# Performance work log

Hardware: AMD Instinct MI355X
Metric: run time of the kernel (lower is better)

The kernel has to match this reference:

```python
import jax, jax.numpy as jnp
import numpy as np
from jax import lax

INPUT_DIM = 512
KERNEL_DIM = 3
HEADS = 8
B, L = 16, 1024


def setup_inputs() -> dict:
    key = jax.random.key(0)
    ks = jax.random.split(key, 4)
    fan = INPUT_DIM * KERNEL_DIM
    std = float(np.sqrt(2.0 / (INPUT_DIM + fan)))  # xavier_normal for conv weight
    x = jax.random.normal(ks[0], (B, INPUT_DIM, L), dtype=jnp.float32)
    w0 = jax.random.normal(ks[1], (INPUT_DIM, INPUT_DIM, KERNEL_DIM), dtype=jnp.float32) * std
    w1 = jax.random.normal(ks[2], (INPUT_DIM, INPUT_DIM, KERNEL_DIM), dtype=jnp.float32) * std
    w2 = jax.random.normal(ks[3], (INPUT_DIM, INPUT_DIM, KERNEL_DIM), dtype=jnp.float32) * std
    b0 = jnp.zeros((INPUT_DIM,), jnp.float32)
    b1 = jnp.zeros((INPUT_DIM,), jnp.float32)
    b2 = jnp.zeros((INPUT_DIM,), jnp.float32)
    return {"x": x, "w0": w0, "b0": b0, "w1": w1, "b1": b1, "w2": w2, "b2": b2}


def _conv1d(x, w, b):
    # x: [B, C, L], w: [O, I, K] -> [B, O, L-K+1] (VALID, stride 1)
    y = lax.conv_general_dilated(x, w, window_strides=(1,), padding='VALID',
                                 dimension_numbers=('NCH', 'OIH', 'NCH'))
    return y + b[None, :, None]


def _multihead_attention(q, k, v, input_dim, heads):
    # q,k,v: [B, D, Lp]; chunk along channel dim == reshape to [B, H, Dh, Lp]
    b, d, lp = q.shape
    dh = d // heads
    qh = q.reshape(b, heads, dh, lp)
    kh = k.reshape(b, heads, dh, lp)
    vh = v.reshape(b, heads, dh, lp)
    scale = 1.0 / np.sqrt(input_dim)  # NOTE: original scales by sqrt(full input_dim)
    scores = jnp.einsum('bhdq,bhdk->bhqk', qh, kh) * scale  # [B,H,Lp,Lp]
    attn = jax.nn.softmax(scores, axis=-1)
    out = jnp.einsum('bhqk,bhdk->bhdq', attn, vh)  # [B,H,Dh,Lp]
    return out.reshape(b, d, lp)


def reference(x, w0, b0, w1, b1, w2, b2):
    q = _conv1d(x, w0, b0)
    k = _conv1d(x, w1, b1)
    v = _conv1d(x, w2, b2)
    return _multihead_attention(q, k, v, INPUT_DIM, HEADS)
```

## Files before the change

kernel.cpp:

```cpp
#include <hip/hip_runtime.h>

#define B_SZ 16
#define CIN  512
#define LIN  1024
#define LP   1022
#define HEADS 8
#define DH    64

typedef __attribute__((ext_vector_type(8))) short bf16x8;
typedef __attribute__((ext_vector_type(4))) float f32x4;

__device__ inline unsigned short f2bf(float f) {
    union { float f; unsigned int u; } c; c.f = f;
    unsigned int r = c.u + 0x7FFF + ((c.u >> 16) & 1);
    return (unsigned short)(r >> 16);
}

__device__ __forceinline__ void gl_lds16(const unsigned short* g, unsigned short* l) {
    __builtin_amdgcn_global_load_lds((const __attribute__((address_space(1))) void*)g,
                                     (__attribute__((address_space(3))) void*)l, 16, 0, 0);
}

#define SWZ(G) ((G) ^ (((G) >> 3) & 7))

__global__ __launch_bounds__(256) void xb_cvt_kernel(const float* __restrict__ x,
                                                     unsigned short* __restrict__ xb) {
    __shared__ float sm[64][68];
    const int t  = threadIdx.x;
    const int l0 = blockIdx.x * 64;
    const int i0 = blockIdx.y * 64;
    const int b  = blockIdx.z;
    const float* S = x + ((size_t)b * CIN + i0) * LIN;

    #pragma unroll
    for (int rr = 0; rr < 4; rr++) {
        int idx = rr * 1024 + t * 4;
        int ii = idx >> 6, lj = idx & 63;
        *(float4*)&sm[ii][lj] = *(const float4*)(S + (size_t)ii * LIN + l0 + lj);
    }
    __syncthreads();

    #pragma unroll
    for (int rr = 0; rr < 4; rr++) {
        int idx = rr * 1024 + t * 4;
        int l = idx >> 6, dj = idx & 63;
        ushort4 h;
        h.x = f2bf(sm[dj + 0][l]);
        h.y = f2bf(sm[dj + 1][l]);
        h.z = f2bf(sm[dj + 2][l]);
        h.w = f2bf(sm[dj + 3][l]);
        *(ushort4*)(xb + ((size_t)b * 1024 + l0 + l) * 512 + i0 + dj) = h;
    }
}

__global__ __launch_bounds__(256) void wb_cvt_kernel(const float* __restrict__ w0,
                                                     const float* __restrict__ w1,
                                                     const float* __restrict__ w2,
                                                     unsigned short* __restrict__ wb) {
    const int kk = blockIdx.y;
    int flat = blockIdx.x * 256 + threadIdx.x;
    int i  = flat & 511;
    int oG = flat >> 9;
    int c  = oG >> 9, o = oG & 511;
    const float* w = (c == 0) ? w0 : (c == 1) ? w1 : w2;
    wb[(size_t)kk * 786432 + flat] = f2bf(w[o * 1536 + i * 3 + kk]);
}

__global__ __launch_bounds__(256) void conv_mfma_kernel(
        const unsigned short* __restrict__ xb,
        const unsigned short* __restrict__ wb,
        const float* __restrict__ b0, const float* __restrict__ b1,
        const float* __restrict__ b2,
        unsigned short* __restrict__ Qt, unsigned short* __restrict__ Kt,
        unsigned short* __restrict__ Vt, float qscale) {
    __shared__ unsigned short smem[16896];
    unsigned short* xs = smem;
    unsigned short* ws = smem + 4224;

    const int t    = threadIdx.x;
    const int wave = t >> 6;
    const int lane = t & 63;
    const int col  = lane & 15;
    const int quad = lane >> 4;
    const int wh   = wave >> 1;
    const int wn   = wave & 1;
    const int l0   = blockIdx.x * 128;
    const int o0   = blockIdx.y * 128;
    const int b    = blockIdx.z;

    f32x4 acc[4][4];
    #pragma unroll
    for (int i = 0; i < 4; i++)
        #pragma unroll
        for (int j = 0; j < 4; j++) acc[i][j] = (f32x4){0.f, 0.f, 0.f, 0.f};

    const unsigned short* xrow = xb + (size_t)b * 1024 * 512;

    for (int ic = 0; ic < 512; ic += 32) {
        __syncthreads();

        #pragma unroll
        for (int j = 0; j < 6; j++) {
            int instr = wave * 6 + j;
            int Gg = SWZ(instr * 64 + lane);
            int p = Gg >> 2, q = Gg & 3;
            int kk = p >> 7, orow = p & 127;
            gl_lds16(wb + ((size_t)(kk * 1536 + o0 + orow)) * 512 + ic + q * 8,
                     ws + instr * 512);
        }
        #pragma unroll
        for (int j = 0; j < 2; j++) {
            int instr = wave * 2 + j;
            int Gg = SWZ(instr * 64 + lane);
            int p = Gg >> 2, q = Gg & 3;
            gl_lds16(xrow + (size_t)(l0 + p) * 512 + ic + q * 8,
                     xs + instr * 512);
        }
        if (t < 8) {
            int row = 128 + (t >> 2), sg = t & 3;
            int gl = l0 + row;
            bf16x8 v = (bf16x8){0, 0, 0, 0, 0, 0, 0, 0};
            if (gl < 1024) v = *(const bf16x8*)(xrow + (size_t)gl * 512 + ic + sg * 8);
            *(bf16x8*)&xs[SWZ(512 + t) * 8] = v;
        }
        __syncthreads();

        #pragma unroll
        for (int kk = 0; kk < 3; kk++) {
            bf16x8 af[4], bfr[4];
            #pragma unroll
            for (int ms = 0; ms < 4; ms++) {
                int G = ((kk * 128 + wh * 64 + ms * 16 + col) << 2) | quad;
                af[ms] = *(const bf16x8*)&ws[SWZ(G) * 8];
            }
            #pragma unroll
            for (int ns = 0; ns < 4; ns++) {
                int G = ((wn * 64 + ns * 16 + col + kk) << 2) | quad;
                bfr[ns] = *(const bf16x8*)&xs[SWZ(G) * 8];
            }
            #pragma unroll
            for (int ms = 0; ms < 4; ms++)
                #pragma unroll
                for (int ns = 0; ns < 4; ns++)
                    acc[ms][ns] = __builtin_amdgcn_mfma_f32_16x16x32_bf16(af[ms], bfr[ns], acc[ms][ns], 0, 0, 0);
        }
    }

    const int c = blockIdx.y >> 2;

    if (c < 2) {
        unsigned short* dst = (c == 0) ? Qt : Kt;
        const float* bias   = (c == 0) ? b0 : b1;
        const float sc      = (c == 0) ? qscale : 1.0f;
        const int h = (((o0 & 511) + wh * 64) >> 6) & 7;
        unsigned short* base = dst + (size_t)(b * 8 + h) * 65536;
        #pragma unroll
        for (int ms = 0; ms < 4; ms++) {
            int ob = (o0 & 511) + wh * 64 + ms * 16 + quad * 4;
            float bv[4];
            #pragma unroll
            for (int r = 0; r < 4; r++) bv[r] = bias[ob + r];
            int d0 = ms * 16 + quad * 4;
            #pragma unroll
            for (int ns = 0; ns < 4; ns++) {
                int l = l0 + wn * 64 + ns * 16 + col;
                ushort4 hv;
                hv.x = f2bf((acc[ms][ns][0] + bv[0]) * sc);
                hv.y = f2bf((acc[ms][ns][1] + bv[1]) * sc);
                hv.z = f2bf((acc[ms][ns][2] + bv[2]) * sc);
                hv.w = f2bf((acc[ms][ns][3] + bv[3]) * sc);
                *(ushort4*)(base + (size_t)l * 64 + d0) = hv;
            }
        }
    } else {
        __syncthreads();
        unsigned short* vt = smem;
        #pragma unroll
        for (int ms = 0; ms < 4; ms++) {
            int ob = (o0 & 511) + wh * 64 + ms * 16 + quad * 4;
            #pragma unroll
            for (int ns = 0; ns < 4; ns++) {
                int lc = wn * 64 + ns * 16 + col;
                #pragma unroll
                for (int r = 0; r < 4; r++)
                    vt[(wh * 64 + ms * 16 + quad * 4 + r) * 132 + lc] =
                        f2bf(acc[ms][ns][r] + b2[ob + r]);
            }
        }
        __syncthreads();
        #pragma unroll
        for (int it = 0; it < 8; it++) {
            int flat = it * 2048 + t * 8;
            int row = flat >> 7, colx = flat & 127;
            bf16x8 v = *(const bf16x8*)&vt[row * 132 + colx];
            int og = (o0 & 511) + row;
            int h = og >> 6, d = og & 63;
            *(bf16x8*)(Vt + ((size_t)(b * 8 + h) * 64 + d) * 1024 + l0 + colx) = v;
        }
    }
}

__global__ __launch_bounds__(256, 4) void attn_kernel(
        const unsigned short* __restrict__ Qt,
        const unsigned short* __restrict__ Kt,
        const unsigned short* __restrict__ Vt,
        float* __restrict__ out) {
    __shared__ unsigned short smem[17408];
    unsigned short* Ks = smem;
    unsigned short* Vs = smem + 4096;
    unsigned short* Ps = smem + 8192;

    const int t    = threadIdx.x;
    const int wave = t >> 6;
    const int lane = t & 63;
    const int col  = lane & 15;
    const int quad = lane >> 4;
    const int qb   = blockIdx.x;
    const int bh   = blockIdx.y;

    const size_t base64 = (size_t)bh * 1024 * 64;
    const int q0w = qb * 128 + wave * 32;

    bf16x8 bq[2][2];
    #pragma unroll
    for (int g = 0; g < 2; g++) {
        const unsigned short* qrow = Qt + base64 + (size_t)(q0w + g * 16 + col) * 64;
        bq[g][0] = *(const bf16x8*)(qrow + quad * 8);
        bq[g][1] = *(const bf16x8*)(qrow + 32 + quad * 8);
    }

    const bf16x8 ones = (bf16x8){0x3F80, 0x3F80, 0x3F80, 0x3F80,
                                 0x3F80, 0x3F80, 0x3F80, 0x3F80};

    f32x4 o[2][4];
    #pragma unroll
    for (int g = 0; g < 2; g++)
        #pragma unroll
        for (int d = 0; d < 4; d++) o[g][d] = (f32x4){0.f, 0.f, 0.f, 0.f};
    f32x4 osum[2];
    osum[0] = (f32x4){0.f, 0.f, 0.f, 0.f};
    osum[1] = (f32x4){0.f, 0.f, 0.f, 0.f};

    const unsigned short* kg0 = Kt + base64;
    const unsigned short* vg  = Vt + base64;
    unsigned short* Pw = Ps + wave * 32 * 72;

    for (int kt = 0; kt < 16; kt++) {
        __syncthreads();

        const unsigned short* kg = kg0 + (size_t)kt * 4096;
        #pragma unroll
        for (int j = 0; j < 2; j++) {
            int i = wave + j * 4;
            int G = SWZ(i * 64 + lane);
            gl_lds16(kg + (size_t)G * 8, Ks + i * 512);
            int p = G >> 3, q = G & 7;
            gl_lds16(vg + (size_t)p * 1024 + kt * 64 + q * 8, Vs + i * 512);
        }
        __syncthreads();

        bf16x8 ak[4][2];
        #pragma unroll
        for (int sub = 0; sub < 4; sub++) {
            int rk = sub * 16 + col;
            ak[sub][0] = *(const bf16x8*)&Ks[SWZ(rk * 8 + quad) * 8];
            ak[sub][1] = *(const bf16x8*)&Ks[SWZ(rk * 8 + 4 + quad) * 8];
        }

        #pragma unroll
        for (int g = 0; g < 2; g++) {
            #pragma unroll
            for (int sub = 0; sub < 4; sub++) {
                f32x4 a = (f32x4){0.f, 0.f, 0.f, 0.f};
                a = __builtin_amdgcn_mfma_f32_16x16x32_bf16(ak[sub][0], bq[g][0], a, 0, 0, 0);
                a = __builtin_amdgcn_mfma_f32_16x16x32_bf16(ak[sub][1], bq[g][1], a, 0, 0, 0);
                unsigned int u[4];
                #pragma unroll
                for (int r = 0; r < 4; r++) {
                    union { float f; unsigned int u; } c;
                    c.f = exp2f(a[r]);
                    u[r] = c.u;
                }
                if (kt == 15 && sub == 3 && quad == 3) {
                    u[2] = 0; u[3] = 0;
                }
                uint2 pk;
                pk.x = (u[0] >> 16) | (u[1] & 0xFFFF0000u);
                pk.y = (u[2] >> 16) | (u[3] & 0xFFFF0000u);
                *(uint2*)&Pw[(g * 16 + col) * 72 + sub * 16 + quad * 4] = pk;
            }
        }

        bf16x8 av[4][2];
        #pragma unroll
        for (int dsub = 0; dsub < 4; dsub++) {
            int rd = dsub * 16 + col;
            av[dsub][0] = *(const bf16x8*)&Vs[SWZ(rd * 8 + quad) * 8];
            av[dsub][1] = *(const bf16x8*)&Vs[SWZ(rd * 8 + 4 + quad) * 8];
        }

        #pragma unroll
        for (int g = 0; g < 2; g++) {
            bf16x8 bp0 = *(const bf16x8*)&Pw[(g * 16 + col) * 72 + quad * 8];
            bf16x8 bp1 = *(const bf16x8*)&Pw[(g * 16 + col) * 72 + 32 + quad * 8];
            #pragma unroll
            for (int dsub = 0; dsub < 4; dsub++) {
                o[g][dsub] = __builtin_amdgcn_mfma_f32_16x16x32_bf16(av[dsub][0], bp0, o[g][dsub], 0, 0, 0);
                o[g][dsub] = __builtin_amdgcn_mfma_f32_16x16x32_bf16(av[dsub][1], bp1, o[g][dsub], 0, 0, 0);
            }
            osum[g] = __builtin_amdgcn_mfma_f32_16x16x32_bf16(ones, bp0, osum[g], 0, 0, 0);
            osum[g] = __builtin_amdgcn_mfma_f32_16x16x32_bf16(ones, bp1, osum[g], 0, 0, 0);
        }
    }

    #pragma unroll
    for (int g = 0; g < 2; g++) {
        int q = q0w + g * 16 + col;
        if (q < LP) {
            float inv = 1.0f / osum[g][0];
            #pragma unroll
            for (int dsub = 0; dsub < 4; dsub++) {
                #pragma unroll
                for (int r = 0; r < 4; r++) {
                    int d = dsub * 16 + quad * 4 + r;
                    out[((size_t)bh * 64 + d) * LP + q] = o[g][dsub][r] * inv;
                }
            }
        }
    }
}

extern "C" void kernel_launch(void* const* d_in, const int* in_sizes, int n_in,
                              void* d_out, int out_size, void* d_ws, size_t ws_size,
                              hipStream_t stream) {
    const float* x  = (const float*)d_in[0];
    const float* w0 = (const float*)d_in[1];
    const float* b0 = (const float*)d_in[2];
    const float* w1 = (const float*)d_in[3];
    const float* b1 = (const float*)d_in[4];
    const float* w2 = (const float*)d_in[5];
    const float* b2 = (const float*)d_in[6];
    float* out = (float*)d_out;

    unsigned short* xbp = (unsigned short*)d_ws;
    unsigned short* wbp = xbp + 8388608;
    unsigned short* Qt  = wbp + 2359296;
    unsigned short* Kt  = Qt + 8388608;
    unsigned short* Vt  = Kt + 8388608;

    const float scale = 0.06375870864f;

    xb_cvt_kernel<<<dim3(16, 8, 16), 256, 0, stream>>>(x, xbp);
    wb_cvt_kernel<<<dim3(3072, 3), 256, 0, stream>>>(w0, w1, w2, wbp);
    conv_mfma_kernel<<<dim3(8, 12, 16), 256, 0, stream>>>(xbp, wbp, b0, b1, b2,
                                                          Qt, Kt, Vt, scale);
    attn_kernel<<<dim3(8, 128), 256, 0, stream>>>(Qt, Kt, Vt, out);
}
```

Before: 242.0 us.

## Double-buffer K/V tiles in attention, remap blocks per XCD, add MFMA priority

The attention kernel now prefetches the next K/V tile into a second LDS buffer while computing on the current one, replacing the two per-iteration __syncthreads with a single waitcnt plus barrier. Block indices are remapped so that all query blocks of a given batch-head land on the same XCD, which should improve L2 reuse of K/V. s_setprio raises wave priority around the MFMA groups. LDS use grows from about 34 KB to 50 KB and the occupancy hint drops from 4 to 3 blocks per CU, so there is less latency hiding from resident waves.

```diff
diff --git a/kernel.cpp b/kernel.cpp
--- a/kernel.cpp
+++ b/kernel.cpp
@@ -200,23 +200,25 @@
     }
 }
 
-__global__ __launch_bounds__(256, 4) void attn_kernel(
+__global__ __launch_bounds__(256, 3) void attn_kernel(
         const unsigned short* __restrict__ Qt,
         const unsigned short* __restrict__ Kt,
         const unsigned short* __restrict__ Vt,
         float* __restrict__ out) {
-    __shared__ unsigned short smem[17408];
-    unsigned short* Ks = smem;
-    unsigned short* Vs = smem + 4096;
-    unsigned short* Ps = smem + 8192;
+    __shared__ unsigned short smem[25600];
+    unsigned short* Ps = smem + 16384;
 
     const int t    = threadIdx.x;
     const int wave = t >> 6;
     const int lane = t & 63;
     const int col  = lane & 15;
     const int quad = lane >> 4;
-    const int qb   = blockIdx.x;
-    const int bh   = blockIdx.y;
+
+    const int lin = blockIdx.y * 8 + blockIdx.x;
+    const int xcd = lin & 7;
+    const int idx = lin >> 3;
+    const int qb  = idx >> 4;
+    const int bh  = xcd * 16 + (idx & 15);
 
     const size_t base64 = (size_t)bh * 1024 * 64;
     const int q0w = qb * 128 + wave * 32;
@@ -245,26 +247,50 @@
     const unsigned short* vg  = Vt + base64;
     unsigned short* Pw = Ps + wave * 32 * 72;
 
+    #pragma unroll
+    for (int j = 0; j < 2; j++) {
+        int i = wave + j * 4;
+        int G = SWZ(i * 64 + lane);
+        gl_lds16(kg0 + (size_t)G * 8, smem + i * 512);
+        int p = G >> 3, q = G & 7;
+        gl_lds16(vg + (size_t)p * 1024 + q * 8, smem + 4096 + i * 512);
+    }
+    asm volatile("s_waitcnt vmcnt(0)" ::: "memory");
+    __builtin_amdgcn_s_barrier();
+    asm volatile("" ::: "memory");
+
+    int cur = 0;
     for (int kt = 0; kt < 16; kt++) {
-        __syncthreads();
-
-        const unsigned short* kg = kg0 + (size_t)kt * 4096;
-        #pragma unroll
-        for (int j = 0; j < 2; j++) {
-            int i = wave + j * 4;
-            int G = SWZ(i * 64 + lane);
-            gl_lds16(kg + (size_t)G * 8, Ks + i * 512);
-            int p = G >> 3, q = G & 7;
-            gl_lds16(vg + (size_t)p * 1024 + kt * 64 + q * 8, Vs + i * 512);
-        }
-        __syncthreads();
+        if (kt < 15) {
+            const unsigned short* kg = kg0 + (size_t)(kt + 1) * 4096;
+            unsigned short* Kb = smem + (cur ^ 1) * 8192;
+            #pragma unroll
+            for (int j = 0; j < 2; j++) {
+                int i = wave + j * 4;
+                int G = SWZ(i * 64 + lane);
+                gl_lds16(kg + (size_t)G * 8, Kb + i * 512);
+                int p = G >> 3, q = G & 7;
+                gl_lds16(vg + (size_t)p * 1024 + (kt + 1) * 64 + q * 8,
+                         Kb + 4096 + i * 512);
+            }
+        }
+
+        const unsigned short* Ksb = smem + cur * 8192;
+        const unsigned short* Vsb = Ksb + 4096;
 
         bf16x8 ak[4][2];
         #pragma unroll
         for (int sub = 0; sub < 4; sub++) {
             int rk = sub * 16 + col;
-            ak[sub][0] = *(const bf16x8*)&Ks[SWZ(rk * 8 + quad) * 8];
-            ak[sub][1] = *(const bf16x8*)&Ks[SWZ(rk * 8 + 4 + quad) * 8];
+            ak[sub][0] = *(const bf16x8*)&Ksb[SWZ(rk * 8 + quad) * 8];
+            ak[sub][1] = *(const bf16x8*)&Ksb[SWZ(rk * 8 + 4 + quad) * 8];
+        }
+        bf16x8 av[4][2];
+        #pragma unroll
+        for (int dsub = 0; dsub < 4; dsub++) {
+            int rd = dsub * 16 + col;
+            av[dsub][0] = *(const bf16x8*)&Vsb[SWZ(rd * 8 + quad) * 8];
+            av[dsub][1] = *(const bf16x8*)&Vsb[SWZ(rd * 8 + 4 + quad) * 8];
         }
 
         #pragma unroll
@@ -272,8 +298,10 @@
             #pragma unroll
             for (int sub = 0; sub < 4; sub++) {
                 f32x4 a = (f32x4){0.f, 0.f, 0.f, 0.f};
+                __builtin_amdgcn_s_setprio(1);
                 a = __builtin_amdgcn_mfma_f32_16x16x32_bf16(ak[sub][0], bq[g][0], a, 0, 0, 0);
                 a = __builtin_amdgcn_mfma_f32_16x16x32_bf16(ak[sub][1], bq[g][1], a, 0, 0, 0);
+                __builtin_amdgcn_s_setprio(0);
                 unsigned int u[4];
                 #pragma unroll
                 for (int r = 0; r < 4; r++) {
@@ -291,18 +319,11 @@
             }
         }
 
-        bf16x8 av[4][2];
-        #pragma unroll
-        for (int dsub = 0; dsub < 4; dsub++) {
-            int rd = dsub * 16 + col;
-            av[dsub][0] = *(const bf16x8*)&Vs[SWZ(rd * 8 + quad) * 8];
-            av[dsub][1] = *(const bf16x8*)&Vs[SWZ(rd * 8 + 4 + quad) * 8];
-        }
-
         #pragma unroll
         for (int g = 0; g < 2; g++) {
             bf16x8 bp0 = *(const bf16x8*)&Pw[(g * 16 + col) * 72 + quad * 8];
             bf16x8 bp1 = *(const bf16x8*)&Pw[(g * 16 + col) * 72 + 32 + quad * 8];
+            __builtin_amdgcn_s_setprio(1);
             #pragma unroll
             for (int dsub = 0; dsub < 4; dsub++) {
                 o[g][dsub] = __builtin_amdgcn_mfma_f32_16x16x32_bf16(av[dsub][0], bp0, o[g][dsub], 0, 0, 0);
@@ -310,7 +331,13 @@
             }
             osum[g] = __builtin_amdgcn_mfma_f32_16x16x32_bf16(ones, bp0, osum[g], 0, 0, 0);
             osum[g] = __builtin_amdgcn_mfma_f32_16x16x32_bf16(ones, bp1, osum[g], 0, 0, 0);
-        }
+            __builtin_amdgcn_s_setprio(0);
+        }
+
+        asm volatile("s_waitcnt vmcnt(0)" ::: "memory");
+        __builtin_amdgcn_s_barrier();
+        asm volatile("" ::: "memory");
+        cur ^= 1;
     }
 
     #pragma unroll
```

After: 242.3 us. No clear change (+0.1%).
